# Kernel tuning notes

Hardware: AMD Instinct MI355X
Metric: run time of the kernel (lower is better)

Reference implementation:

```python
import jax, jax.numpy as jnp
import numpy as np
from jax import lax

DIM = 384
NE = 8
TOPK = 2
HID = 4 * DIM
N, H, W = 32, 32, 32
EPS = 1e-6


def setup_inputs() -> dict:
    key = jax.random.key(0)
    ks = jax.random.split(key, 12)
    s = 0.02
    return {
        "input": jax.random.normal(ks[0], (N, DIM, H, W), dtype=jnp.float32),
        "dw_w": jax.random.normal(ks[1], (DIM, 1, 7, 7), dtype=jnp.float32) * s,
        "dw_b": jnp.zeros((DIM,), dtype=jnp.float32),
        "ln_g": jnp.ones((DIM,), dtype=jnp.float32),
        "ln_b": jnp.zeros((DIM,), dtype=jnp.float32),
        "gate_w": jax.random.normal(ks[2], (NE, DIM), dtype=jnp.float32) * s,
        "w1": jax.random.normal(ks[3], (NE, DIM, HID), dtype=jnp.float32) * s,
        "b1": jnp.zeros((NE, HID), dtype=jnp.float32),
        "w2": jax.random.normal(ks[4], (NE, HID, DIM), dtype=jnp.float32) * s,
        "b2": jnp.zeros((NE, DIM), dtype=jnp.float32),
        "layer_scale": jnp.ones((DIM, 1, 1), dtype=jnp.float32) * 1e-6,
    }


def reference(input, dw_w, dw_b, ln_g, ln_b, gate_w, w1, b1, w2, b2, layer_scale):
    # depthwise 7x7 conv, padding 3, groups=DIM  (NCHW)
    x = lax.conv_general_dilated(
        input, dw_w, window_strides=(1, 1), padding=((3, 3), (3, 3)),
        dimension_numbers=("NCHW", "OIHW", "NCHW"), feature_group_count=DIM,
    ) + dw_b[None, :, None, None]
    # permute to NHWC, layernorm over C with eps=1e-6
    x = jnp.transpose(x, (0, 2, 3, 1))
    mu = jnp.mean(x, axis=-1, keepdims=True)
    var = jnp.mean(jnp.square(x - mu), axis=-1, keepdims=True)
    x = (x - mu) * lax.rsqrt(var + EPS) * ln_g + ln_b

    x_flat = x.reshape(-1, DIM)  # [T, C]
    logits = x_flat @ gate_w.T   # [T, NE]
    topv, topi = lax.top_k(logits, TOPK)
    weights = jax.nn.softmax(topv, axis=-1)  # [T, K]

    # combine: out[t] = sum_e gate_e[t] * Expert_e(x_flat[t]), gate nonzero only for top-k
    out = jnp.zeros_like(x_flat)
    for e in range(NE):
        we = jnp.sum(jnp.where(topi == e, weights, 0.0), axis=-1)  # [T]
        h = jax.nn.gelu(x_flat @ w1[e] + b1[e], approximate=False)
        y = h @ w2[e] + b2[e]
        out = out + y * we[:, None]

    out = out.reshape(N, H, W, DIM)
    out = jnp.transpose(out, (0, 3, 1, 2))  # back to NCHW
    out = layer_scale[None] * out           # [C,1,1] broadcast
    # stochastic_depth prob 0.0 -> identity
    return input + out
```

## Files before the change

kernel.cpp:

```cpp
#include <hip/hip_runtime.h>
#include <hip/hip_bf16.h>
#include <hip/hip_fp8.h>

typedef __attribute__((ext_vector_type(4))) float  f32x4;
typedef __attribute__((ext_vector_type(8))) unsigned short u16x8;
typedef __attribute__((ext_vector_type(4))) unsigned short u16x4;
typedef long long f8x8;

#define DIM 384
#define NE 8
#define HID 1536
#define NB 32
#define HW 1024
#define T_TOK 32768

__device__ __forceinline__ unsigned short f2bf(float f) {
    unsigned int u = __float_as_uint(f);
    u = (u + 0x7fffu + ((u >> 16) & 1u)) >> 16;
    return (unsigned short)u;
}
__device__ __forceinline__ float bf2f(unsigned short u) {
    return __uint_as_float((unsigned int)u << 16);
}
__device__ __forceinline__ unsigned char f2fp8(float f) {
    __hip_fp8_e4m3 h(f);
    return (unsigned char)h.__x;
}

__global__ __launch_bounds__(256) void k_transpose8(const float* __restrict__ src,
                                                    unsigned char* __restrict__ dst,
                                                    int R, int C) {
    int b = blockIdx.x;
    int ctiles = C >> 5;
    int rtiles = R >> 5;
    int ct = b % ctiles;
    int rt = (b / ctiles) % rtiles;
    int e  = b / (ctiles * rtiles);
    __shared__ float t[32][33];
    int tid = threadIdx.x;
    const float* s = src + (size_t)e * R * C;
    unsigned char* d = dst + (size_t)e * C * R;
#pragma unroll
    for (int k = 0; k < 4; ++k) {
        int idx = k * 256 + tid;
        int rr = idx >> 5, cc = idx & 31;
        t[rr][cc] = s[(size_t)(rt * 32 + rr) * C + ct * 32 + cc];
    }
    __syncthreads();
    int cc = tid >> 3, r4 = tid & 7;
    unsigned int pk = 0;
#pragma unroll
    for (int i = 0; i < 4; ++i)
        pk |= (unsigned int)f2fp8(t[r4 * 4 + i][cc]) << (8 * i);
    *(unsigned int*)&d[(size_t)(ct * 32 + cc) * R + rt * 32 + r4 * 4] = pk;
}

__global__ __launch_bounds__(256) void k_conv(const float* __restrict__ in,
                                              const float* __restrict__ dw_w,
                                              const float* __restrict__ dw_b,
                                              float* __restrict__ xconv) {
    int nc = blockIdx.x;
    int c = nc % DIM;
    __shared__ float tile[38 * 38];
    __shared__ float wt[49];
    const float* plane = in + (size_t)nc * HW;
    int tid = threadIdx.x;
    if (tid < 49) wt[tid] = dw_w[c * 49 + tid];
    for (int idx = tid; idx < 38 * 38; idx += 256) {
        int ty = idx / 38, tx = idx % 38;
        int ih = ty - 3, iw = tx - 3;
        float v = 0.f;
        if ((unsigned)ih < 32u && (unsigned)iw < 32u) v = plane[ih * 32 + iw];
        tile[idx] = v;
    }
    __syncthreads();
    float bias = dw_b[c];
    int w = tid & 31, h0 = (tid >> 5) << 2;
    float acc[4] = {bias, bias, bias, bias};
#pragma unroll
    for (int iy = 0; iy < 10; ++iy) {
        float r[7];
#pragma unroll
        for (int dx = 0; dx < 7; ++dx) r[dx] = tile[(h0 + iy) * 38 + w + dx];
#pragma unroll
        for (int o = 0; o < 4; ++o) {
            int dy = iy - o;
            if (dy >= 0 && dy < 7) {
                float a = 0.f;
#pragma unroll
                for (int dx = 0; dx < 7; ++dx) a += r[dx] * wt[dy * 7 + dx];
                acc[o] += a;
            }
        }
    }
    float* outp = xconv + (size_t)nc * HW;
#pragma unroll
    for (int o = 0; o < 4; ++o) outp[(h0 + o) * 32 + w] = acc[o];
}

__global__ __launch_bounds__(256) void k_ln_gate(const float* __restrict__ xconv,
                                                 const float* __restrict__ ln_g,
                                                 const float* __restrict__ ln_b,
                                                 const float* __restrict__ gate_w,
                                                 unsigned char* __restrict__ lnout,
                                                 int* __restrict__ lists,
                                                 float* __restrict__ wgts,
                                                 int* __restrict__ counts) {
    __shared__ float xs[32][385];
    __shared__ float gw[8][384];
    __shared__ float gls[384], bls[384];
    __shared__ int hcnt[8], hbase[8];
    __shared__ int lexp[32][2];
    __shared__ int lpos[32][2];
    __shared__ float lw[32][2];

    int b = blockIdx.x;
    int n = b >> 5;
    int hw0 = (b & 31) << 5;
    int tid = threadIdx.x;

    for (int i = tid; i < 384; i += 256) { gls[i] = ln_g[i]; bls[i] = ln_b[i]; }
    for (int i = tid; i < 8 * 384; i += 256) gw[i / 384][i % 384] = gate_w[i];
    if (tid < 8) hcnt[tid] = 0;

    const float* base = xconv + (size_t)n * DIM * HW + hw0;
#pragma unroll
    for (int k = 0; k < 48; ++k) {
        int idx = k * 256 + tid;
        int c = idx >> 5, j = idx & 31;
        xs[j][c] = base[(size_t)c * HW + j];
    }
    __syncthreads();

    int tok = tid >> 3, jj = tid & 7;
    float sum = 0.f, sq = 0.f;
#pragma unroll
    for (int k = 0; k < 48; ++k) {
        float v = xs[tok][jj + 8 * k];
        sum += v; sq += v * v;
    }
#pragma unroll
    for (int m = 1; m < 8; m <<= 1) { sum += __shfl_xor(sum, m); sq += __shfl_xor(sq, m); }
    float mu = sum * (1.f / 384.f);
    float var = sq * (1.f / 384.f) - mu * mu;
    float rstd = rsqrtf(var + 1e-6f);

    int tglob = n * HW + hw0 + tok;
    float p[8] = {0, 0, 0, 0, 0, 0, 0, 0};
#pragma unroll
    for (int k = 0; k < 48; ++k) {
        int c = jj + 8 * k;
        float v = (xs[tok][c] - mu) * rstd * gls[c] + bls[c];
        lnout[(size_t)tglob * DIM + c] = f2fp8(v);
#pragma unroll
        for (int e = 0; e < 8; ++e) p[e] += v * gw[e][c];
    }
#pragma unroll
    for (int e = 0; e < 8; ++e)
#pragma unroll
        for (int m = 1; m < 8; m <<= 1) p[e] += __shfl_xor(p[e], m);

    if (jj == 0) {
        int i0 = 0; float v0 = p[0];
#pragma unroll
        for (int e = 1; e < 8; ++e) if (p[e] > v0) { v0 = p[e]; i0 = e; }
        int i1 = -1; float v1 = -1e30f;
#pragma unroll
        for (int e = 0; e < 8; ++e) if (e != i0 && p[e] > v1) { v1 = p[e]; i1 = e; }
        float w0 = 1.f / (1.f + __expf(v1 - v0));
        float w1 = 1.f - w0;
        lexp[tok][0] = i0; lexp[tok][1] = i1;
        lw[tok][0] = w0;  lw[tok][1] = w1;
        lpos[tok][0] = atomicAdd(&hcnt[i0], 1);
        lpos[tok][1] = atomicAdd(&hcnt[i1], 1);
    }
    __syncthreads();
    if (tid < 8) hbase[tid] = atomicAdd(&counts[tid], hcnt[tid]);
    __syncthreads();
    if (jj == 0) {
#pragma unroll
        for (int s = 0; s < 2; ++s) {
            int e = lexp[tok][s];
            int pos = hbase[e] + lpos[tok][s];
            lists[e * T_TOK + pos] = (tglob << 1) | s;
            wgts[e * T_TOK + pos] = lw[tok][s];
        }
    }
}

__global__ __launch_bounds__(512, 1) void k_moe(const unsigned char* __restrict__ ln,
                                                const unsigned char* __restrict__ w1t,
                                                const unsigned char* __restrict__ w2t,
                                                const float* __restrict__ b1,
                                                const float* __restrict__ b2,
                                                const int* __restrict__ lists,
                                                const float* __restrict__ wgts,
                                                const int* __restrict__ counts,
                                                unsigned short* __restrict__ y0,
                                                unsigned short* __restrict__ y1) {
    int e    = blockIdx.x & 7;
    int tile = blockIdx.x >> 3;
    int cnt = counts[e];
    if (tile * 128 >= cnt) return;

    __shared__ unsigned char X[128][400];
    __shared__ unsigned char Hs[128][136];
    __shared__ int   ents[128];
    __shared__ float wrow[128];

    int tid = threadIdx.x;
    if (tid < 128) {
        int idx = tile * 128 + tid;
        if (idx < cnt) { ents[tid] = lists[e * T_TOK + idx]; wrow[tid] = wgts[e * T_TOK + idx]; }
        else           { ents[tid] = -1;                     wrow[tid] = 0.f; }
    }
    __syncthreads();

    {
        int row = tid >> 2, q = tid & 3;
        int ent = ents[row];
        int tok = (ent < 0) ? 0 : (ent >> 1);
        const u16x8* src = (const u16x8*)(ln + (size_t)tok * DIM);
#pragma unroll
        for (int r = 0; r < 6; ++r)
            *(u16x8*)&X[row][(q + r * 4) * 16] = __builtin_nontemporal_load(&src[q + r * 4]);
    }
    __syncthreads();

    int wid = tid >> 6;
    int lane = tid & 63;
    int lr = lane & 15;
    int lq = lane >> 4;

    const unsigned char* pw1 = w1t + ((size_t)e * HID + wid * 16 + lr) * DIM + lq * 8;
    const unsigned char* pw2 = w2t + ((size_t)e * DIM + wid * 48 + lr) * HID + lq * 8;

    f32x4 Yacc[3][8] = {};

    f8x8 wall[12];
#pragma unroll
    for (int k = 0; k < 12; ++k) wall[k] = *(const f8x8*)(pw1 + k * 32);

    for (int hc = 0; hc < 12; ++hc) {
        f8x8 vall[12];
#pragma unroll
        for (int t = 0; t < 12; ++t) {
            int nj = t % 3, k2 = t / 3;
            vall[t] = *(const f8x8*)(pw2 + (size_t)nj * 16 * HID + hc * 128 + k2 * 32);
        }
        f32x4 bv = *(const f32x4*)&b1[e * HID + hc * 128 + wid * 16 + lq * 4];
        f32x4 Hf[8];
#pragma unroll
        for (int m = 0; m < 8; ++m) Hf[m] = bv;
        __builtin_amdgcn_s_setprio(1);
#pragma unroll
        for (int k = 0; k < 12; ++k) {
#pragma unroll
            for (int m = 0; m < 8; ++m) {
                f8x8 a = *(const f8x8*)&X[m * 16 + lr][k * 32 + lq * 8];
                Hf[m] = __builtin_amdgcn_mfma_f32_16x16x32_fp8_fp8(wall[k], a, Hf[m], 0, 0, 0);
            }
        }
        __builtin_amdgcn_s_setprio(0);
        if (hc < 11) {
            const unsigned char* pn = pw1 + (size_t)(hc + 1) * 128 * DIM;
#pragma unroll
            for (int k = 0; k < 12; ++k) wall[k] = *(const f8x8*)(pn + k * 32);
        }
#pragma unroll
        for (int m = 0; m < 8; ++m) {
            unsigned int pk = 0;
#pragma unroll
            for (int r = 0; r < 4; ++r) {
                float v = Hf[m][r];
                float t = v * fmaf(v * v, -0.07135481627f, -1.5957691216f);
                float g = v * __builtin_amdgcn_rcpf(1.f + __expf(t));
                pk |= (unsigned int)f2fp8(g) << (8 * r);
            }
            *(unsigned int*)&Hs[m * 16 + lr][wid * 16 + lq * 4] = pk;
        }
        asm volatile("s_waitcnt lgkmcnt(0)" ::: "memory");
        __builtin_amdgcn_s_barrier();
        __builtin_amdgcn_sched_barrier(0);
        __builtin_amdgcn_s_setprio(1);
#pragma unroll
        for (int k2 = 0; k2 < 4; ++k2) {
#pragma unroll
            for (int m = 0; m < 8; ++m) {
                f8x8 h = *(const f8x8*)&Hs[m * 16 + lr][k2 * 32 + lq * 8];
#pragma unroll
                for (int nj = 0; nj < 3; ++nj) {
                    Yacc[nj][m] = __builtin_amdgcn_mfma_f32_16x16x32_fp8_fp8(vall[k2 * 3 + nj], h, Yacc[nj][m], 0, 0, 0);
                }
            }
        }
        __builtin_amdgcn_s_setprio(0);
        asm volatile("s_waitcnt lgkmcnt(0)" ::: "memory");
        __builtin_amdgcn_s_barrier();
        __builtin_amdgcn_sched_barrier(0);
    }

    f32x4 b2v[3];
#pragma unroll
    for (int nj = 0; nj < 3; ++nj)
        b2v[nj] = *(const f32x4*)&b2[e * DIM + wid * 48 + nj * 16 + lq * 4];
#pragma unroll
    for (int m = 0; m < 8; ++m) {
        int row = m * 16 + lr;
        int ent = ents[row];
        if (ent >= 0) {
            float wv = wrow[row];
            int tok = ent >> 1;
            unsigned short* yb = (ent & 1) ? y1 : y0;
#pragma unroll
            for (int nj = 0; nj < 3; ++nj) {
                u16x4 pk;
#pragma unroll
                for (int r = 0; r < 4; ++r)
                    pk[r] = f2bf((Yacc[nj][m][r] + b2v[nj][r]) * wv);
                *(u16x4*)(yb + (size_t)tok * DIM + wid * 48 + nj * 16 + lq * 4) = pk;
            }
        }
    }
}

__global__ __launch_bounds__(256) void k_final(const float* __restrict__ input,
                                               const float* __restrict__ ls,
                                               const unsigned short* __restrict__ y0,
                                               const unsigned short* __restrict__ y1,
                                               float* __restrict__ out) {
    int b = blockIdx.x;
    int ct = b % 12;
    int hwt = (b / 12) % 32;
    int n = b / (12 * 32);
    int c0 = ct * 32, hw0 = hwt * 32;
    __shared__ float t[32][33];
    int tid = threadIdx.x;
    int t0 = n * HW + hw0;
#pragma unroll
    for (int k = 0; k < 2; ++k) {
        int idx = k * 256 + tid;
        int tl = idx >> 4, pr = idx & 15;
        size_t o = (size_t)(t0 + tl) * DIM + c0 + pr * 2;
        unsigned int a = *(const unsigned int*)(y0 + o);
        unsigned int c = *(const unsigned int*)(y1 + o);
        t[tl][pr * 2]     = bf2f((unsigned short)a) + bf2f((unsigned short)c);
        t[tl][pr * 2 + 1] = bf2f((unsigned short)(a >> 16)) + bf2f((unsigned short)(c >> 16));
    }
    __syncthreads();
#pragma unroll
    for (int k = 0; k < 4; ++k) {
        int idx = k * 256 + tid;
        int cl = idx >> 5, j = idx & 31;
        size_t o = ((size_t)n * DIM + c0 + cl) * HW + hw0 + j;
        out[o] = input[o] + ls[c0 + cl] * t[j][cl];
    }
}

extern "C" void kernel_launch(void* const* d_in, const int* in_sizes, int n_in,
                              void* d_out, int out_size, void* d_ws, size_t ws_size,
                              hipStream_t stream) {
    const float* input  = (const float*)d_in[0];
    const float* dw_w   = (const float*)d_in[1];
    const float* dw_b   = (const float*)d_in[2];
    const float* ln_g   = (const float*)d_in[3];
    const float* ln_b   = (const float*)d_in[4];
    const float* gate_w = (const float*)d_in[5];
    const float* w1     = (const float*)d_in[6];
    const float* b1     = (const float*)d_in[7];
    const float* w2     = (const float*)d_in[8];
    const float* b2     = (const float*)d_in[9];
    const float* lscale = (const float*)d_in[10];

    const size_t SZ_PLANE = (size_t)NB * DIM * HW * 4;
    const size_t SZ_YBF   = (size_t)T_TOK * DIM * 2;
    const size_t SZ_LNB   = (size_t)T_TOK * DIM;
    const size_t SZ_W1    = (size_t)NE * DIM * HID;
    char* ws = (char*)d_ws;
    float* xconv = (float*)(ws + 0);
    unsigned short* y0 = (unsigned short*)(ws + 0);
    unsigned short* y1 = (unsigned short*)(ws + SZ_YBF);
    unsigned char* lnb = (unsigned char*)(ws + SZ_PLANE);
    unsigned char* w1t = (unsigned char*)(ws + SZ_PLANE + SZ_LNB);
    unsigned char* w2t = (unsigned char*)(ws + SZ_PLANE + SZ_LNB + SZ_W1);
    int*   lists  = (int*)(ws + SZ_PLANE + SZ_LNB + 2 * SZ_W1);
    float* wgt    = (float*)(ws + SZ_PLANE + SZ_LNB + 2 * SZ_W1 + 1048576);
    int*   counts = (int*)(ws + SZ_PLANE + SZ_LNB + 2 * SZ_W1 + 2 * 1048576);
    const size_t needed = SZ_PLANE + SZ_LNB + 2 * SZ_W1 + 2 * 1048576 + 256;
    if (ws_size < needed) return;

    hipMemsetAsync(counts, 0, 32, stream);
    k_transpose8<<<8 * 12 * 48, 256, 0, stream>>>(w1, w1t, DIM, HID);
    k_transpose8<<<8 * 48 * 12, 256, 0, stream>>>(w2, w2t, HID, DIM);
    k_conv<<<NB * DIM, 256, 0, stream>>>(input, dw_w, dw_b, xconv);
    k_ln_gate<<<T_TOK / 32, 256, 0, stream>>>(xconv, ln_g, ln_b, gate_w, lnb, lists, wgt, counts);
    k_moe<<<NE * 256, 512, 0, stream>>>(lnb, w1t, w2t, b1, b2, lists, wgt, counts, y0, y1);
    k_final<<<NB * 32 * 12, 256, 0, stream>>>(input, lscale, y0, y1, (float*)d_out);
}
```

Before: 408.2 us.

## Restructure MoE kernel to keep expert hidden activations in registers, dropping LDS

Rewrites the expert FFN kernel so each wave independently handles 32 tokens across the full hidden dimension. The GELU output stays in registers and feeds the second matmul directly as an MFMA operand, which removes the shared-memory staging and per-chunk block barriers. A new transpose kernel repacks w2 into a chunked fp8 layout so these per-wave loads are contiguous. In exchange, every wave now streams the whole expert's weights from cache. That is roughly four times the weight traffic per token compared with sharing across a 128-token block, and the large register accumulators limit occupancy.

```diff
diff --git a/kernel.cpp b/kernel.cpp
--- a/kernel.cpp
+++ b/kernel.cpp
@@ -25,6 +25,10 @@
 __device__ __forceinline__ unsigned char f2fp8(float f) {
     __hip_fp8_e4m3 h(f);
     return (unsigned char)h.__x;
+}
+__device__ __forceinline__ float gelu_f(float v) {
+    float zz = v * fmaf(v * v, -0.07135481627f, -1.5957691216f);
+    return v * __builtin_amdgcn_rcpf(1.f + __expf(zz));
 }
 
 __global__ __launch_bounds__(256) void k_transpose8(const float* __restrict__ src,
@@ -53,6 +57,31 @@
     for (int i = 0; i < 4; ++i)
         pk |= (unsigned int)f2fp8(t[r4 * 4 + i][cc]) << (8 * i);
     *(unsigned int*)&d[(size_t)(ct * 32 + cc) * R + rt * 32 + r4 * 4] = pk;
+}
+
+__global__ __launch_bounds__(256) void k_transw2(const float* __restrict__ src,
+                                                 unsigned char* __restrict__ dst) {
+    int b = blockIdx.x;
+    int ct = b % 12;
+    int rt = (b / 12) % 48;
+    int e  = b / (12 * 48);
+    __shared__ float t[32][33];
+    int tid = threadIdx.x;
+    const float* s = src + (size_t)e * HID * DIM;
+#pragma unroll
+    for (int k = 0; k < 4; ++k) {
+        int idx = k * 256 + tid;
+        int rr = idx >> 5, cc = idx & 31;
+        t[rr][cc] = s[(size_t)(rt * 32 + rr) * DIM + ct * 32 + cc];
+    }
+    __syncthreads();
+    int cc = tid >> 3, r4 = tid & 7;
+    unsigned int pk = 0;
+#pragma unroll
+    for (int i = 0; i < 4; ++i)
+        pk |= (unsigned int)f2fp8(t[r4 * 4 + i][cc]) << (8 * i);
+    size_t off = (((size_t)e * 48 + rt) * DIM + ct * 32 + cc) * 32 + 8 * (r4 & 3) + 4 * (r4 >> 2);
+    *(unsigned int*)&dst[off] = pk;
 }
 
 __global__ __launch_bounds__(256) void k_conv(const float* __restrict__ in,
@@ -188,9 +217,9 @@
     }
 }
 
-__global__ __launch_bounds__(512, 1) void k_moe(const unsigned char* __restrict__ ln,
+__global__ __launch_bounds__(256, 1) void k_moe(const unsigned char* __restrict__ ln,
                                                 const unsigned char* __restrict__ w1t,
-                                                const unsigned char* __restrict__ w2t,
+                                                const unsigned char* __restrict__ w2p,
                                                 const float* __restrict__ b1,
                                                 const float* __restrict__ b2,
                                                 const int* __restrict__ lists,
@@ -203,123 +232,98 @@
     int cnt = counts[e];
     if (tile * 128 >= cnt) return;
 
-    __shared__ unsigned char X[128][400];
-    __shared__ unsigned char Hs[128][136];
-    __shared__ int   ents[128];
-    __shared__ float wrow[128];
-
-    int tid = threadIdx.x;
-    if (tid < 128) {
-        int idx = tile * 128 + tid;
-        if (idx < cnt) { ents[tid] = lists[e * T_TOK + idx]; wrow[tid] = wgts[e * T_TOK + idx]; }
-        else           { ents[tid] = -1;                     wrow[tid] = 0.f; }
-    }
-    __syncthreads();
-
+    int tid = threadIdx.x;
+    int wid = tid >> 6;
+    int l   = tid & 63;
+    int lr  = l & 15;
+    int lq  = l >> 4;
+
+    int base = tile * 128 + wid * 32;
+    int idx0 = base + lr;
+    int idx1 = idx0 + 16;
+    int ent0 = (idx0 < cnt) ? lists[e * T_TOK + idx0] : -1;
+    int ent1 = (idx1 < cnt) ? lists[e * T_TOK + idx1] : -1;
+    float wv0 = (idx0 < cnt) ? wgts[e * T_TOK + idx0] : 0.f;
+    float wv1 = (idx1 < cnt) ? wgts[e * T_TOK + idx1] : 0.f;
+    int tok0 = (ent0 < 0) ? 0 : (ent0 >> 1);
+    int tok1 = (ent1 < 0) ? 0 : (ent1 >> 1);
+
+    f8x8 xf0[12], xf1[12];
     {
-        int row = tid >> 2, q = tid & 3;
-        int ent = ents[row];
-        int tok = (ent < 0) ? 0 : (ent >> 1);
-        const u16x8* src = (const u16x8*)(ln + (size_t)tok * DIM);
-#pragma unroll
-        for (int r = 0; r < 6; ++r)
-            *(u16x8*)&X[row][(q + r * 4) * 16] = __builtin_nontemporal_load(&src[q + r * 4]);
-    }
-    __syncthreads();
-
-    int wid = tid >> 6;
-    int lane = tid & 63;
-    int lr = lane & 15;
-    int lq = lane >> 4;
-
-    const unsigned char* pw1 = w1t + ((size_t)e * HID + wid * 16 + lr) * DIM + lq * 8;
-    const unsigned char* pw2 = w2t + ((size_t)e * DIM + wid * 48 + lr) * HID + lq * 8;
-
-    f32x4 Yacc[3][8] = {};
-
-    f8x8 wall[12];
-#pragma unroll
-    for (int k = 0; k < 12; ++k) wall[k] = *(const f8x8*)(pw1 + k * 32);
-
-    for (int hc = 0; hc < 12; ++hc) {
-        f8x8 vall[12];
-#pragma unroll
-        for (int t = 0; t < 12; ++t) {
-            int nj = t % 3, k2 = t / 3;
-            vall[t] = *(const f8x8*)(pw2 + (size_t)nj * 16 * HID + hc * 128 + k2 * 32);
-        }
-        f32x4 bv = *(const f32x4*)&b1[e * HID + hc * 128 + wid * 16 + lq * 4];
-        f32x4 Hf[8];
-#pragma unroll
-        for (int m = 0; m < 8; ++m) Hf[m] = bv;
-        __builtin_amdgcn_s_setprio(1);
-#pragma unroll
-        for (int k = 0; k < 12; ++k) {
-#pragma unroll
-            for (int m = 0; m < 8; ++m) {
-                f8x8 a = *(const f8x8*)&X[m * 16 + lr][k * 32 + lq * 8];
-                Hf[m] = __builtin_amdgcn_mfma_f32_16x16x32_fp8_fp8(wall[k], a, Hf[m], 0, 0, 0);
-            }
-        }
-        __builtin_amdgcn_s_setprio(0);
-        if (hc < 11) {
-            const unsigned char* pn = pw1 + (size_t)(hc + 1) * 128 * DIM;
-#pragma unroll
-            for (int k = 0; k < 12; ++k) wall[k] = *(const f8x8*)(pn + k * 32);
-        }
-#pragma unroll
-        for (int m = 0; m < 8; ++m) {
-            unsigned int pk = 0;
-#pragma unroll
-            for (int r = 0; r < 4; ++r) {
-                float v = Hf[m][r];
-                float t = v * fmaf(v * v, -0.07135481627f, -1.5957691216f);
-                float g = v * __builtin_amdgcn_rcpf(1.f + __expf(t));
-                pk |= (unsigned int)f2fp8(g) << (8 * r);
-            }
-            *(unsigned int*)&Hs[m * 16 + lr][wid * 16 + lq * 4] = pk;
-        }
-        asm volatile("s_waitcnt lgkmcnt(0)" ::: "memory");
-        __builtin_amdgcn_s_barrier();
-        __builtin_amdgcn_sched_barrier(0);
-        __builtin_amdgcn_s_setprio(1);
-#pragma unroll
-        for (int k2 = 0; k2 < 4; ++k2) {
-#pragma unroll
-            for (int m = 0; m < 8; ++m) {
-                f8x8 h = *(const f8x8*)&Hs[m * 16 + lr][k2 * 32 + lq * 8];
-#pragma unroll
-                for (int nj = 0; nj < 3; ++nj) {
-                    Yacc[nj][m] = __builtin_amdgcn_mfma_f32_16x16x32_fp8_fp8(vall[k2 * 3 + nj], h, Yacc[nj][m], 0, 0, 0);
-                }
-            }
-        }
-        __builtin_amdgcn_s_setprio(0);
-        asm volatile("s_waitcnt lgkmcnt(0)" ::: "memory");
-        __builtin_amdgcn_s_barrier();
-        __builtin_amdgcn_sched_barrier(0);
-    }
-
-    f32x4 b2v[3];
-#pragma unroll
-    for (int nj = 0; nj < 3; ++nj)
-        b2v[nj] = *(const f32x4*)&b2[e * DIM + wid * 48 + nj * 16 + lq * 4];
-#pragma unroll
-    for (int m = 0; m < 8; ++m) {
-        int row = m * 16 + lr;
-        int ent = ents[row];
-        if (ent >= 0) {
-            float wv = wrow[row];
-            int tok = ent >> 1;
-            unsigned short* yb = (ent & 1) ? y1 : y0;
-#pragma unroll
-            for (int nj = 0; nj < 3; ++nj) {
-                u16x4 pk;
-#pragma unroll
-                for (int r = 0; r < 4; ++r)
-                    pk[r] = f2bf((Yacc[nj][m][r] + b2v[nj][r]) * wv);
-                *(u16x4*)(yb + (size_t)tok * DIM + wid * 48 + nj * 16 + lq * 4) = pk;
-            }
+        const unsigned char* px0 = ln + (size_t)tok0 * DIM + lq * 8;
+        const unsigned char* px1 = ln + (size_t)tok1 * DIM + lq * 8;
+#pragma unroll
+        for (int ks = 0; ks < 12; ++ks) {
+            xf0[ks] = *(const f8x8*)(px0 + ks * 32);
+            xf1[ks] = *(const f8x8*)(px1 + ks * 32);
+        }
+    }
+
+    const unsigned char* pa0 = w1t + ((size_t)e * HID + lr) * DIM + lq * 8;
+    const unsigned char* pa1 = pa0 + (size_t)16 * DIM;
+    const unsigned char* pv = w2p + (((size_t)e * 48) * DIM + lr) * 32 + lq * 8;
+    const float* pb1 = b1 + e * HID + lq * 4;
+
+    f32x4 Yacc[24][2] = {};
+
+#pragma unroll 2
+    for (int c = 0; c < 48; ++c) {
+        f8x8 wa0[12], wa1[12];
+#pragma unroll
+        for (int ks = 0; ks < 12; ++ks) {
+            wa0[ks] = *(const f8x8*)(pa0 + ks * 32);
+            wa1[ks] = *(const f8x8*)(pa1 + ks * 32);
+        }
+        f8x8 va[24];
+#pragma unroll
+        for (int nj = 0; nj < 24; ++nj)
+            va[nj] = *(const f8x8*)(pv + nj * 512);
+        f32x4 bv0 = *(const f32x4*)(pb1);
+        f32x4 bv1 = *(const f32x4*)(pb1 + 16);
+        f32x4 H00 = bv0, H01 = bv0, H10 = bv1, H11 = bv1;
+#pragma unroll
+        for (int ks = 0; ks < 12; ++ks) {
+            H00 = __builtin_amdgcn_mfma_f32_16x16x32_fp8_fp8(wa0[ks], xf0[ks], H00, 0, 0, 0);
+            H01 = __builtin_amdgcn_mfma_f32_16x16x32_fp8_fp8(wa0[ks], xf1[ks], H01, 0, 0, 0);
+            H10 = __builtin_amdgcn_mfma_f32_16x16x32_fp8_fp8(wa1[ks], xf0[ks], H10, 0, 0, 0);
+            H11 = __builtin_amdgcn_mfma_f32_16x16x32_fp8_fp8(wa1[ks], xf1[ks], H11, 0, 0, 0);
+        }
+        unsigned int lo0 = 0, hi0 = 0, lo1 = 0, hi1 = 0;
+#pragma unroll
+        for (int i = 0; i < 4; ++i) {
+            lo0 |= (unsigned int)f2fp8(gelu_f(H00[i])) << (8 * i);
+            hi0 |= (unsigned int)f2fp8(gelu_f(H10[i])) << (8 * i);
+            lo1 |= (unsigned int)f2fp8(gelu_f(H01[i])) << (8 * i);
+            hi1 |= (unsigned int)f2fp8(gelu_f(H11[i])) << (8 * i);
+        }
+        f8x8 bf0 = (f8x8)((((unsigned long long)hi0) << 32) | lo0);
+        f8x8 bf1 = (f8x8)((((unsigned long long)hi1) << 32) | lo1);
+#pragma unroll
+        for (int nj = 0; nj < 24; ++nj) {
+            Yacc[nj][0] = __builtin_amdgcn_mfma_f32_16x16x32_fp8_fp8(va[nj], bf0, Yacc[nj][0], 0, 0, 0);
+            Yacc[nj][1] = __builtin_amdgcn_mfma_f32_16x16x32_fp8_fp8(va[nj], bf1, Yacc[nj][1], 0, 0, 0);
+        }
+        pa0 += (size_t)32 * DIM;
+        pa1 += (size_t)32 * DIM;
+        pv  += (size_t)DIM * 32;
+        pb1 += 32;
+    }
+
+#pragma unroll
+    for (int t = 0; t < 2; ++t) {
+        int ent = t ? ent1 : ent0;
+        if (ent < 0) continue;
+        float wv = t ? wv1 : wv0;
+        int tok = ent >> 1;
+        unsigned short* yb = (ent & 1) ? y1 : y0;
+#pragma unroll
+        for (int nj = 0; nj < 24; ++nj) {
+            f32x4 b2v = *(const f32x4*)&b2[e * DIM + nj * 16 + lq * 4];
+            u16x4 pk;
+#pragma unroll
+            for (int i = 0; i < 4; ++i)
+                pk[i] = f2bf((Yacc[nj][t][i] + b2v[i]) * wv);
+            *(u16x4*)(yb + (size_t)tok * DIM + nj * 16 + lq * 4) = pk;
         }
     }
 }
@@ -382,7 +386,7 @@
     unsigned short* y1 = (unsigned short*)(ws + SZ_YBF);
     unsigned char* lnb = (unsigned char*)(ws + SZ_PLANE);
     unsigned char* w1t = (unsigned char*)(ws + SZ_PLANE + SZ_LNB);
-    unsigned char* w2t = (unsigned char*)(ws + SZ_PLANE + SZ_LNB + SZ_W1);
+    unsigned char* w2p = (unsigned char*)(ws + SZ_PLANE + SZ_LNB + SZ_W1);
     int*   lists  = (int*)(ws + SZ_PLANE + SZ_LNB + 2 * SZ_W1);
     float* wgt    = (float*)(ws + SZ_PLANE + SZ_LNB + 2 * SZ_W1 + 1048576);
     int*   counts = (int*)(ws + SZ_PLANE + SZ_LNB + 2 * SZ_W1 + 2 * 1048576);
@@ -391,9 +395,9 @@
 
     hipMemsetAsync(counts, 0, 32, stream);
     k_transpose8<<<8 * 12 * 48, 256, 0, stream>>>(w1, w1t, DIM, HID);
-    k_transpose8<<<8 * 48 * 12, 256, 0, stream>>>(w2, w2t, HID, DIM);
+    k_transw2<<<8 * 48 * 12, 256, 0, stream>>>(w2, w2p);
     k_conv<<<NB * DIM, 256, 0, stream>>>(input, dw_w, dw_b, xconv);
     k_ln_gate<<<T_TOK / 32, 256, 0, stream>>>(xconv, ln_g, ln_b, gate_w, lnb, lists, wgt, counts);
-    k_moe<<<NE * 256, 512, 0, stream>>>(lnb, w1t, w2t, b1, b2, lists, wgt, counts, y0, y1);
+    k_moe<<<NE * 512, 256, 0, stream>>>(lnb, w1t, w2p, b1, b2, lists, wgt, counts, y0, y1);
     k_final<<<NB * 32 * 12, 256, 0, stream>>>(input, lscale, y0, y1, (float*)d_out);
 }
```

Measured after the change: 806.4 us. +97.6%, slower.
